# Kernel tuning notes

Measured on AMD Instinct MI355X. Metric: run time of the kernel, lower is better.

Reference implementation:

```python
import jax, jax.numpy as jnp
import numpy as np

N_NODES = 50000
N_EDGES = 600000
DIM = 128
N_HEADS = 3
EDGE_VOCAB = 22754
NEG_SLOPE = 0.2


def setup_inputs() -> dict:
    key = jax.random.key(0)
    ks = jax.random.split(key, 12)
    s = 1.0 / np.sqrt(DIM)
    return {
        "x": jax.random.normal(ks[0], (N_NODES, DIM), dtype=jnp.float32),
        "edge_index": jax.random.randint(ks[1], (2, N_EDGES), 0, N_NODES, dtype=jnp.int64),
        "edge_ids": jax.random.randint(ks[2], (N_EDGES,), 0, EDGE_VOCAB, dtype=jnp.int64),
        "ddi_weight": jax.random.uniform(ks[3], (N_EDGES,), dtype=jnp.float32),
        "W_lin": jax.random.normal(ks[4], (DIM, DIM), dtype=jnp.float32) * s,
        "b_lin": jnp.zeros((DIM,), dtype=jnp.float32),
        "edge_emb": jax.random.normal(ks[5], (EDGE_VOCAB, 1), dtype=jnp.float32) * 0.1,
        "W_heads": jax.random.normal(ks[6], (N_HEADS, DIM, DIM), dtype=jnp.float32) * s,
        "att_src": jax.random.normal(ks[7], (N_HEADS, DIM), dtype=jnp.float32) * s,
        "att_dst": jax.random.normal(ks[8], (N_HEADS, DIM), dtype=jnp.float32) * s,
        "bias_heads": jnp.zeros((N_HEADS, DIM), dtype=jnp.float32),
    }


def _gat_head(x, src, dst, ew, W, a_src, a_dst, bias):
    # x: [N, D] (already passed through shared lin), ew: [E] scalar edge weights
    h = x @ W                                   # [N, D]
    e = jax.nn.leaky_relu(
        (h @ a_src)[src] + (h @ a_dst)[dst], NEG_SLOPE)   # [E]
    # segment softmax over destination nodes
    e_max = jax.ops.segment_max(e, dst, num_segments=N_NODES)   # [N]
    e_exp = jnp.exp(e - e_max[dst])                              # [E]
    denom = jax.ops.segment_sum(e_exp, dst, num_segments=N_NODES)
    alpha = e_exp / jnp.maximum(denom[dst], 1e-16)               # [E]
    msg = (alpha * ew)[:, None] * h[src]                         # [E, D]
    return jax.ops.segment_sum(msg, dst, num_segments=N_NODES) + bias


def reference(x, edge_index, edge_ids, ddi_weight, W_lin, b_lin, edge_emb,
              W_heads, att_src, att_dst, bias_heads):
    x = x @ W_lin + b_lin                         # shared linear projection
    ew = edge_emb[edge_ids, 0] - ddi_weight        # [E]
    src, dst = edge_index[0], edge_index[1]
    out = jnp.zeros_like(x)
    for hix in range(N_HEADS):                     # small fixed head count
        out = out + _gat_head(x, src, dst, ew, W_heads[hix],
                              att_src[hix], att_dst[hix], bias_heads[hix])
    return out / N_HEADS
```

## Files before the change

### kernel.cpp

```cpp
#include <hip/hip_runtime.h>
#include <math.h>

#define NN 50000
#define NE 600000
#define D 128
#define NH 3
#define CAP 64
#define EDGE_BLOCKS ((NE + 255) / 256)
#define MFMA_BLOCKS ((NN + 63) / 64)

typedef short bf16x8 __attribute__((ext_vector_type(8)));
typedef _Float16 f16x8 __attribute__((ext_vector_type(8)));
typedef float f32x4 __attribute__((ext_vector_type(4)));

__device__ __forceinline__ unsigned short f2b(float f) {
  unsigned int u = __float_as_uint(f);
  u += 0x7FFF + ((u >> 16) & 1);
  return (unsigned short)(u >> 16);
}
__device__ __forceinline__ float blo(unsigned int u) {
  return __uint_as_float(u << 16);
}
__device__ __forceinline__ float bhi(unsigned int u) {
  return __uint_as_float(u & 0xffff0000u);
}
__device__ __forceinline__ unsigned short f2h(float f) {
  _Float16 t = (_Float16)f;
  return *(unsigned short*)&t;
}

__global__ __launch_bounds__(256) void pack_scatter2(const float* __restrict__ W_lin,
                                                     const float* __restrict__ W_heads,
                                                     const float* __restrict__ att_src,
                                                     const float* __restrict__ att_dst,
                                                     const float* __restrict__ b_lin,
                                                     const float* __restrict__ bias_heads,
                                                     const int* __restrict__ ei,
                                                     const int* __restrict__ eid,
                                                     const float* __restrict__ ddi,
                                                     const float* __restrict__ emb,
                                                     uint4* __restrict__ Bpack,
                                                     uint4* __restrict__ Wpack3,
                                                     float* __restrict__ sbuf,
                                                     float* __restrict__ bcomb2,
                                                     int* __restrict__ counts,
                                                     unsigned int* __restrict__ slots8) {
  const int bx = blockIdx.x;
  const int tid = threadIdx.x;
  if (bx < EDGE_BLOCKS) {
    int e = bx * 256 + tid;
    if (e < NE) {
      int src = ei[e], dst = ei[NE + e];
      int idx = atomicAdd(&counts[dst], 1);
      idx = idx < CAP ? idx : CAP - 1;
      float ew = emb[eid[e]] - ddi[e];
      slots8[dst * CAP + idx] = (unsigned int)src | ((unsigned int)f2b(ew) << 16);
    }
    return;
  }
  const int pb = bx - EDGE_BLOCKS;
  if (pb < 8) {
    int r = pb * 256 + tid;
    int nt = r >> 8, s = (r >> 6) & 3, q = (r >> 4) & 3, n0 = r & 15;
    int kbase = s * 32 + q * 8;
    int n = nt * 16 + n0;
    unsigned int w[4];
    #pragma unroll
    for (int p = 0; p < 4; ++p) {
      unsigned short lo = f2b(W_lin[(kbase + 2 * p) * D + n]);
      unsigned short hi = f2b(W_lin[(kbase + 2 * p + 1) * D + n]);
      w[p] = (unsigned int)lo | ((unsigned int)hi << 16);
    }
    Bpack[r] = make_uint4(w[0], w[1], w[2], w[3]);
  } else if (pb < 32) {
    int u = (pb - 8) * 256 + tid;
    int h = u >> 11, r = u & 2047;
    int nt = r >> 8, s = (r >> 6) & 3, q = (r >> 4) & 3, n0 = r & 15;
    int kbase = s * 32 + q * 8;
    int n = nt * 16 + n0;
    const float* W = W_heads + (size_t)h * D * D;
    unsigned int w[4];
    #pragma unroll
    for (int p = 0; p < 4; ++p) {
      unsigned short lo = f2h(W[(kbase + 2 * p) * D + n]);
      unsigned short hi = f2h(W[(kbase + 2 * p + 1) * D + n]);
      w[p] = (unsigned int)lo | ((unsigned int)hi << 16);
    }
    Wpack3[h * 2048 + r] = make_uint4(w[0], w[1], w[2], w[3]);
  } else if (pb < 35) {
    const int h = pb - 32;
    __shared__ float wha_s[128], wha_d[128], scs[128], scd[128];
    {
      int m = tid & 127;
      const float* W = W_heads + (size_t)h * D * D + m * D;
      const float* a = (tid < 128) ? (att_src + h * D) : (att_dst + h * D);
      float acc = 0.f;
      for (int n = 0; n < D; ++n) acc += W[n] * a[n];
      if (tid < 128) wha_s[m] = acc; else wha_d[m] = acc;
    }
    __syncthreads();
    {
      int k = tid & 127;
      const float* wl = W_lin + k * D;
      const float* wha = (tid < 128) ? wha_s : wha_d;
      float acc = 0.f;
      for (int m = 0; m < D; ++m) acc += wl[m] * wha[m];
      if (tid < 128) scs[k] = acc; else scd[k] = acc;
    }
    __syncthreads();
    if (tid < 2) {
      const float* wha = tid ? wha_d : wha_s;
      float a = 0.f;
      for (int k = 0; k < D; ++k) a += b_lin[k] * wha[k];
      sbuf[h * 2 + tid] = a;
    }
    {
      int s = (tid >> 6) & 3, q = (tid >> 4) & 3, n0 = tid & 15;
      int kbase = s * 32 + q * 8;
      bool mine = (n0 < 6) && ((n0 >> 1) == h);
      bool zero = (h == 0) && (n0 >= 6);
      if (mine || zero) {
        float vals[8];
        #pragma unroll
        for (int j = 0; j < 8; ++j)
          vals[j] = zero ? 0.f : ((n0 & 1) ? scd[kbase + j] : scs[kbase + j]);
        unsigned int w[4];
        #pragma unroll
        for (int p = 0; p < 4; ++p)
          w[p] = (unsigned int)f2b(vals[2 * p]) | ((unsigned int)f2b(vals[2 * p + 1]) << 16);
        Bpack[2048 + tid] = make_uint4(w[0], w[1], w[2], w[3]);
      }
    }
  } else {
    if (tid < D)
      bcomb2[tid] = (bias_heads[tid] + bias_heads[D + tid] + bias_heads[2 * D + tid]) * (1.f / 3.f);
  }
}

__global__ __launch_bounds__(256) void mfma_x(const float* __restrict__ x,
                                              const uint4* __restrict__ Bpack,
                                              const float* __restrict__ b_lin,
                                              const float* __restrict__ sbuf,
                                              unsigned short* __restrict__ xb,
                                              float* __restrict__ s_src4,
                                              float* __restrict__ s_dst4) {
  const int row0 = blockIdx.x * 64;
  const int tid = threadIdx.x;
  __shared__ __align__(16) unsigned short As[64][136];
  #pragma unroll
  for (int it = 0; it < 8; ++it) {
    int idx = tid + it * 256;
    int m = idx >> 5, k4 = idx & 31;
    int row = row0 + m;
    float4 v = make_float4(0.f, 0.f, 0.f, 0.f);
    if (row < NN) v = ((const float4*)(x + (size_t)row * D))[k4];
    uint2 pk;
    pk.x = (unsigned int)f2b(v.x) | ((unsigned int)f2b(v.y) << 16);
    pk.y = (unsigned int)f2b(v.z) | ((unsigned int)f2b(v.w) << 16);
    *((uint2*)&As[m][k4 * 4]) = pk;
  }
  __syncthreads();
  const int wv = tid >> 6;
  const int lane = tid & 63;
  const int n0 = lane & 15, q = lane >> 4;
  const int boff = q * 16 + n0;
  const bf16x8* Bp = (const bf16x8*)Bpack;

  bf16x8 a4[4];
  #pragma unroll
  for (int s = 0; s < 4; ++s)
    a4[s] = *(const bf16x8*)&As[wv * 16 + n0][s * 32 + q * 8];

  f32x4 acc[9];
  #pragma unroll
  for (int nt = 0; nt < 9; ++nt) acc[nt] = (f32x4){0.f, 0.f, 0.f, 0.f};

  #pragma unroll
  for (int s = 0; s < 4; ++s) {
    #pragma unroll
    for (int nt = 0; nt < 9; ++nt) {
      bf16x8 b = Bp[(nt * 4 + s) * 64 + boff];
      acc[nt] = __builtin_amdgcn_mfma_f32_16x16x32_bf16(a4[s], b, acc[nt], 0, 0, 0);
    }
  }
  __syncthreads();
  #pragma unroll
  for (int nt = 0; nt < 8; ++nt) {
    int col = nt * 16 + n0;
    float bv = b_lin[col];
    #pragma unroll
    for (int r = 0; r < 4; ++r)
      As[wv * 16 + q * 4 + r][col] = f2b(acc[nt][r] + bv);
  }
  if (n0 < 6) {
    float sb = sbuf[n0];
    float* Sout = (n0 & 1) ? s_dst4 : s_src4;
    #pragma unroll
    for (int r = 0; r < 4; ++r) {
      int row = row0 + wv * 16 + q * 4 + r;
      if (row < NN) Sout[row * 4 + (n0 >> 1)] = acc[8][r] + sb;
    }
  }
  __syncthreads();
  #pragma unroll
  for (int i = 0; i < 4; ++i) {
    int idx = tid + i * 256;
    int row = idx >> 4, c16 = idx & 15;
    int grow = row0 + row;
    if (grow < NN)
      *((uint4*)&xb[(size_t)grow * D + c16 * 8]) = *((const uint4*)&As[row][c16 * 8]);
  }
}

__global__ __launch_bounds__(512) void gfin(const int* __restrict__ counts,
                                            const unsigned int* __restrict__ slots8,
                                            const float4* __restrict__ s_src4,
                                            const float4* __restrict__ s_dst4,
                                            const unsigned short* __restrict__ xb,
                                            const uint4* __restrict__ Wpack3,
                                            const float* __restrict__ bcomb2,
                                            float* __restrict__ out) {
  const int row0 = blockIdx.x * 64;
  const int tid = threadIdx.x;
  const int wv = tid >> 6;
  const int lane = tid & 63;
  __shared__ __align__(16) _Float16 Acc[64][392];

  const int hf = lane >> 5;
  const int c = (lane & 31) * 4;
  for (int i = 0; i < 8; ++i) {
    const int m = wv * 8 + i;
    const int dst = row0 + m;
    if (dst < NN) {
      int cnt = counts[dst];
      cnt = cnt < CAP ? cnt : CAP;
      const int beg = dst * CAP;
      const int end = beg + cnt;
      float4 sd = s_dst4[dst];
      float a0[4] = {0.f, 0.f, 0.f, 0.f};
      float a1[4] = {0.f, 0.f, 0.f, 0.f};
      float a2[4] = {0.f, 0.f, 0.f, 0.f};
      float d0 = 0.f, d1 = 0.f, d2 = 0.f;
      int s = beg + hf;
      for (; s + 2 < end; s += 4) {
        unsigned int seA = slots8[s];
        unsigned int seB = slots8[s + 2];
        int srcA = seA & 0xffffu, srcB = seB & 0xffffu;
        float ewA = bhi(seA), ewB = bhi(seB);
        float4 ssA = s_src4[srcA];
        float4 ssB = s_src4[srcB];
        uint2 ua = *(const uint2*)&xb[(size_t)srcA * D + c];
        uint2 ub = *(const uint2*)&xb[(size_t)srcB * D + c];
        float vA0 = ssA.x + sd.x, vA1 = ssA.y + sd.y, vA2 = ssA.z + sd.z;
        float vB0 = ssB.x + sd.x, vB1 = ssB.y + sd.y, vB2 = ssB.z + sd.z;
        vA0 = vA0 > 0.f ? vA0 : 0.2f * vA0;
        vA1 = vA1 > 0.f ? vA1 : 0.2f * vA1;
        vA2 = vA2 > 0.f ? vA2 : 0.2f * vA2;
        vB0 = vB0 > 0.f ? vB0 : 0.2f * vB0;
        vB1 = vB1 > 0.f ? vB1 : 0.2f * vB1;
        vB2 = vB2 > 0.f ? vB2 : 0.2f * vB2;
        float pA0 = __expf(vA0), pA1 = __expf(vA1), pA2 = __expf(vA2);
        float pB0 = __expf(vB0), pB1 = __expf(vB1), pB2 = __expf(vB2);
        float wa0 = pA0 * ewA, wa1 = pA1 * ewA, wa2 = pA2 * ewA;
        float wb0 = pB0 * ewB, wb1 = pB1 * ewB, wb2 = pB2 * ewB;
        float xA[4] = {blo(ua.x), bhi(ua.x), blo(ua.y), bhi(ua.y)};
        float xB[4] = {blo(ub.x), bhi(ub.x), blo(ub.y), bhi(ub.y)};
        #pragma unroll
        for (int j = 0; j < 4; ++j) {
          a0[j] += wa0 * xA[j] + wb0 * xB[j];
          a1[j] += wa1 * xA[j] + wb1 * xB[j];
          a2[j] += wa2 * xA[j] + wb2 * xB[j];
        }
        d0 += pA0 + pB0;
        d1 += pA1 + pB1;
        d2 += pA2 + pB2;
      }
      if (s < end) {
        unsigned int seA = slots8[s];
        int srcA = seA & 0xffffu;
        float ewA = bhi(seA);
        float4 ssA = s_src4[srcA];
        uint2 ua = *(const uint2*)&xb[(size_t)srcA * D + c];
        float vA0 = ssA.x + sd.x, vA1 = ssA.y + sd.y, vA2 = ssA.z + sd.z;
        vA0 = vA0 > 0.f ? vA0 : 0.2f * vA0;
        vA1 = vA1 > 0.f ? vA1 : 0.2f * vA1;
        vA2 = vA2 > 0.f ? vA2 : 0.2f * vA2;
        float pA0 = __expf(vA0), pA1 = __expf(vA1), pA2 = __expf(vA2);
        float w0 = pA0 * ewA, w1 = pA1 * ewA, w2 = pA2 * ewA;
        float xA[4] = {blo(ua.x), bhi(ua.x), blo(ua.y), bhi(ua.y)};
        #pragma unroll
        for (int j = 0; j < 4; ++j) {
          a0[j] += w0 * xA[j];
          a1[j] += w1 * xA[j];
          a2[j] += w2 * xA[j];
        }
        d0 += pA0; d1 += pA1; d2 += pA2;
      }
      #pragma unroll
      for (int j = 0; j < 4; ++j) {
        a0[j] += __shfl_xor(a0[j], 32, 64);
        a1[j] += __shfl_xor(a1[j], 32, 64);
        a2[j] += __shfl_xor(a2[j], 32, 64);
      }
      d0 += __shfl_xor(d0, 32, 64);
      d1 += __shfl_xor(d1, 32, 64);
      d2 += __shfl_xor(d2, 32, 64);
      if (hf == 0) {
        float r0 = 1.f / (3.f * fmaxf(d0, 1e-16f));
        float r1 = 1.f / (3.f * fmaxf(d1, 1e-16f));
        float r2 = 1.f / (3.f * fmaxf(d2, 1e-16f));
        uint2 o;
        o.x = (unsigned int)f2h(a0[0] * r0) | ((unsigned int)f2h(a0[1] * r0) << 16);
        o.y = (unsigned int)f2h(a0[2] * r0) | ((unsigned int)f2h(a0[3] * r0) << 16);
        *(uint2*)&Acc[m][c] = o;
        o.x = (unsigned int)f2h(a1[0] * r1) | ((unsigned int)f2h(a1[1] * r1) << 16);
        o.y = (unsigned int)f2h(a1[2] * r1) | ((unsigned int)f2h(a1[3] * r1) << 16);
        *(uint2*)&Acc[m][D + c] = o;
        o.x = (unsigned int)f2h(a2[0] * r2) | ((unsigned int)f2h(a2[1] * r2) << 16);
        o.y = (unsigned int)f2h(a2[2] * r2) | ((unsigned int)f2h(a2[3] * r2) << 16);
        *(uint2*)&Acc[m][2 * D + c] = o;
      }
    }
  }
  __syncthreads();

  const int n0 = lane & 15, q = lane >> 4;
  const int rw = wv & 3;
  const int cb = wv >> 2;
  const int boff = q * 16 + n0;
  f32x4 o4[4];
  #pragma unroll
  for (int nt = 0; nt < 4; ++nt) o4[nt] = (f32x4){0.f, 0.f, 0.f, 0.f};

  #pragma unroll
  for (int ck = 0; ck < NH; ++ck) {
    f16x8 af[4];
    #pragma unroll
    for (int s = 0; s < 4; ++s)
      af[s] = *(const f16x8*)&Acc[rw * 16 + n0][ck * D + s * 32 + q * 8];
    const f16x8* Bp = (const f16x8*)(Wpack3 + ck * 2048);
    #pragma unroll
    for (int s = 0; s < 4; ++s) {
      #pragma unroll
      for (int nt = 0; nt < 4; ++nt) {
        int NT = cb * 4 + nt;
        f16x8 b = Bp[(NT * 4 + s) * 64 + boff];
        o4[nt] = __builtin_amdgcn_mfma_f32_16x16x32_f16(af[s], b, o4[nt], 0, 0, 0);
      }
    }
  }
  #pragma unroll
  for (int nt = 0; nt < 4; ++nt) {
    int col = cb * 64 + nt * 16 + n0;
    float bv = bcomb2[col];
    #pragma unroll
    for (int r = 0; r < 4; ++r) {
      int row = row0 + rw * 16 + q * 4 + r;
      if (row < NN) out[(size_t)row * D + col] = o4[nt][r] + bv;
    }
  }
}

extern "C" void kernel_launch(void* const* d_in, const int* in_sizes, int n_in,
                              void* d_out, int out_size, void* d_ws, size_t ws_size,
                              hipStream_t stream) {
  const float* x          = (const float*)d_in[0];
  const int*   ei         = (const int*)d_in[1];
  const int*   eid        = (const int*)d_in[2];
  const float* ddi        = (const float*)d_in[3];
  const float* W_lin      = (const float*)d_in[4];
  const float* b_lin      = (const float*)d_in[5];
  const float* emb        = (const float*)d_in[6];
  const float* W_heads    = (const float*)d_in[7];
  const float* att_src    = (const float*)d_in[8];
  const float* att_dst    = (const float*)d_in[9];
  const float* bias_heads = (const float*)d_in[10];
  float* out = (float*)d_out;

  uint4*  Bpack  = (uint4*)d_ws;
  uint4*  Wpack3 = Bpack + 2304;
  unsigned short* xb = (unsigned short*)(Wpack3 + NH * 2048);
  unsigned int* slots8 = (unsigned int*)(xb + (size_t)NN * D);
  float*  sbuf   = (float*)(slots8 + (size_t)NN * CAP);
  float*  bcomb2 = sbuf + 8;
  float*  s_src4 = bcomb2 + 128;
  float*  s_dst4 = s_src4 + (size_t)NN * 4;
  int*    counts = (int*)(s_dst4 + (size_t)NN * 4);

  hipMemsetAsync(counts, 0, (size_t)NN * sizeof(int), stream);
  pack_scatter2<<<EDGE_BLOCKS + 36, 256, 0, stream>>>(
      W_lin, W_heads, att_src, att_dst, b_lin, bias_heads, ei, eid, ddi, emb,
      Bpack, Wpack3, sbuf, bcomb2, counts, slots8);
  mfma_x<<<MFMA_BLOCKS, 256, 0, stream>>>(x, Bpack, b_lin, sbuf, xb,
                                          s_src4, s_dst4);
  gfin<<<MFMA_BLOCKS, 512, 0, stream>>>(counts, slots8, (const float4*)s_src4,
                                        (const float4*)s_dst4, xb, Wpack3,
                                        bcomb2, out);
}
```

Baseline: 242.3 us.

## Split fused gather+GEMM into per-node gather kernel and separate MFMA GEMM

Splits the fused gather-and-project kernel into two kernels. The first is a one-wavefront-per-destination gather that writes per-head aggregated features as fp16 to global memory. The second is a tiled MFMA GEMM that reads those features back and applies the combined weights. It also folds log2(e) into the attention score weights so the kernel can use exp2f instead of __expf. The aim is better load balance and occupancy for the irregular gather, at the cost of an extra global round trip of about 38 MB for the intermediate features and one more launch.

```diff
diff --git a/kernel.cpp b/kernel.cpp
--- a/kernel.cpp
+++ b/kernel.cpp
@@ -8,6 +8,7 @@
 #define CAP 64
 #define EDGE_BLOCKS ((NE + 255) / 256)
 #define MFMA_BLOCKS ((NN + 63) / 64)
+#define LOG2E 1.44269504088896340736f
 
 typedef short bf16x8 __attribute__((ext_vector_type(8)));
 typedef _Float16 f16x8 __attribute__((ext_vector_type(8)));
@@ -105,14 +106,14 @@
       const float* wha = (tid < 128) ? wha_s : wha_d;
       float acc = 0.f;
       for (int m = 0; m < D; ++m) acc += wl[m] * wha[m];
-      if (tid < 128) scs[k] = acc; else scd[k] = acc;
+      if (tid < 128) scs[k] = acc * LOG2E; else scd[k] = acc * LOG2E;
     }
     __syncthreads();
     if (tid < 2) {
       const float* wha = tid ? wha_d : wha_s;
       float a = 0.f;
       for (int k = 0; k < D; ++k) a += b_lin[k] * wha[k];
-      sbuf[h * 2 + tid] = a;
+      sbuf[h * 2 + tid] = a * LOG2E;
     }
     {
       int s = (tid >> 6) & 3, q = (tid >> 4) & 3, n0 = tid & 15;
@@ -212,151 +213,158 @@
   }
 }
 
-__global__ __launch_bounds__(512) void gfin(const int* __restrict__ counts,
-                                            const unsigned int* __restrict__ slots8,
-                                            const float4* __restrict__ s_src4,
-                                            const float4* __restrict__ s_dst4,
-                                            const unsigned short* __restrict__ xb,
-                                            const uint4* __restrict__ Wpack3,
-                                            const float* __restrict__ bcomb2,
-                                            float* __restrict__ out) {
+__global__ __launch_bounds__(64) void gather12(const int* __restrict__ counts,
+                                               const unsigned int* __restrict__ slots8,
+                                               const float4* __restrict__ s_src4,
+                                               const float4* __restrict__ s_dst4,
+                                               const unsigned short* __restrict__ xb,
+                                               unsigned short* __restrict__ accb) {
+  const int dst = blockIdx.x;
+  const int lane = threadIdx.x;
+  const int hf = lane >> 5;
+  const int c = (lane & 31) * 4;
+  int cnt = counts[dst];
+  cnt = cnt < CAP ? cnt : CAP;
+  const int beg = dst * CAP;
+  const int end = beg + cnt;
+  float4 sd = s_dst4[dst];
+  float a0[4] = {0.f, 0.f, 0.f, 0.f};
+  float a1[4] = {0.f, 0.f, 0.f, 0.f};
+  float a2[4] = {0.f, 0.f, 0.f, 0.f};
+  float d0 = 0.f, d1 = 0.f, d2 = 0.f;
+  int s = beg + hf;
+  for (; s + 2 < end; s += 4) {
+    unsigned int seA = slots8[s];
+    unsigned int seB = slots8[s + 2];
+    int srcA = seA & 0xffffu, srcB = seB & 0xffffu;
+    float ewA = bhi(seA), ewB = bhi(seB);
+    float4 ssA = s_src4[srcA];
+    float4 ssB = s_src4[srcB];
+    uint2 ua = *(const uint2*)&xb[(size_t)srcA * D + c];
+    uint2 ub = *(const uint2*)&xb[(size_t)srcB * D + c];
+    float vA0 = ssA.x + sd.x, vA1 = ssA.y + sd.y, vA2 = ssA.z + sd.z;
+    float vB0 = ssB.x + sd.x, vB1 = ssB.y + sd.y, vB2 = ssB.z + sd.z;
+    vA0 = vA0 > 0.f ? vA0 : 0.2f * vA0;
+    vA1 = vA1 > 0.f ? vA1 : 0.2f * vA1;
+    vA2 = vA2 > 0.f ? vA2 : 0.2f * vA2;
+    vB0 = vB0 > 0.f ? vB0 : 0.2f * vB0;
+    vB1 = vB1 > 0.f ? vB1 : 0.2f * vB1;
+    vB2 = vB2 > 0.f ? vB2 : 0.2f * vB2;
+    float pA0 = exp2f(vA0), pA1 = exp2f(vA1), pA2 = exp2f(vA2);
+    float pB0 = exp2f(vB0), pB1 = exp2f(vB1), pB2 = exp2f(vB2);
+    float wa0 = pA0 * ewA, wa1 = pA1 * ewA, wa2 = pA2 * ewA;
+    float wb0 = pB0 * ewB, wb1 = pB1 * ewB, wb2 = pB2 * ewB;
+    float xA[4] = {blo(ua.x), bhi(ua.x), blo(ua.y), bhi(ua.y)};
+    float xB[4] = {blo(ub.x), bhi(ub.x), blo(ub.y), bhi(ub.y)};
+    #pragma unroll
+    for (int j = 0; j < 4; ++j) {
+      a0[j] += wa0 * xA[j] + wb0 * xB[j];
+      a1[j] += wa1 * xA[j] + wb1 * xB[j];
+      a2[j] += wa2 * xA[j] + wb2 * xB[j];
+    }
+    d0 += pA0 + pB0;
+    d1 += pA1 + pB1;
+    d2 += pA2 + pB2;
+  }
+  if (s < end) {
+    unsigned int seA = slots8[s];
+    int srcA = seA & 0xffffu;
+    float ewA = bhi(seA);
+    float4 ssA = s_src4[srcA];
+    uint2 ua = *(const uint2*)&xb[(size_t)srcA * D + c];
+    float vA0 = ssA.x + sd.x, vA1 = ssA.y + sd.y, vA2 = ssA.z + sd.z;
+    vA0 = vA0 > 0.f ? vA0 : 0.2f * vA0;
+    vA1 = vA1 > 0.f ? vA1 : 0.2f * vA1;
+    vA2 = vA2 > 0.f ? vA2 : 0.2f * vA2;
+    float pA0 = exp2f(vA0), pA1 = exp2f(vA1), pA2 = exp2f(vA2);
+    float w0 = pA0 * ewA, w1 = pA1 * ewA, w2 = pA2 * ewA;
+    float xA[4] = {blo(ua.x), bhi(ua.x), blo(ua.y), bhi(ua.y)};
+    #pragma unroll
+    for (int j = 0; j < 4; ++j) {
+      a0[j] += w0 * xA[j];
+      a1[j] += w1 * xA[j];
+      a2[j] += w2 * xA[j];
+    }
+    d0 += pA0; d1 += pA1; d2 += pA2;
+  }
+  #pragma unroll
+  for (int j = 0; j < 4; ++j) {
+    a0[j] += __shfl_xor(a0[j], 32, 64);
+    a1[j] += __shfl_xor(a1[j], 32, 64);
+    a2[j] += __shfl_xor(a2[j], 32, 64);
+  }
+  d0 += __shfl_xor(d0, 32, 64);
+  d1 += __shfl_xor(d1, 32, 64);
+  d2 += __shfl_xor(d2, 32, 64);
+  if (hf == 0) {
+    float r0 = 1.f / (3.f * fmaxf(d0, 1e-16f));
+    float r1 = 1.f / (3.f * fmaxf(d1, 1e-16f));
+    float r2 = 1.f / (3.f * fmaxf(d2, 1e-16f));
+    unsigned short* base = accb + (size_t)dst * (NH * D);
+    uint2 o;
+    o.x = (unsigned int)f2h(a0[0] * r0) | ((unsigned int)f2h(a0[1] * r0) << 16);
+    o.y = (unsigned int)f2h(a0[2] * r0) | ((unsigned int)f2h(a0[3] * r0) << 16);
+    *(uint2*)&base[c] = o;
+    o.x = (unsigned int)f2h(a1[0] * r1) | ((unsigned int)f2h(a1[1] * r1) << 16);
+    o.y = (unsigned int)f2h(a1[2] * r1) | ((unsigned int)f2h(a1[3] * r1) << 16);
+    *(uint2*)&base[D + c] = o;
+    o.x = (unsigned int)f2h(a2[0] * r2) | ((unsigned int)f2h(a2[1] * r2) << 16);
+    o.y = (unsigned int)f2h(a2[2] * r2) | ((unsigned int)f2h(a2[3] * r2) << 16);
+    *(uint2*)&base[2 * D + c] = o;
+  }
+}
+
+__global__ __launch_bounds__(256) void final_gemm16(const unsigned short* __restrict__ accb,
+                                                    const uint4* __restrict__ Wpack3,
+                                                    const float* __restrict__ bcomb2,
+                                                    float* __restrict__ out) {
   const int row0 = blockIdx.x * 64;
   const int tid = threadIdx.x;
+  __shared__ __align__(16) _Float16 Af[64][136];
   const int wv = tid >> 6;
   const int lane = tid & 63;
-  __shared__ __align__(16) _Float16 Acc[64][392];
-
-  const int hf = lane >> 5;
-  const int c = (lane & 31) * 4;
-  for (int i = 0; i < 8; ++i) {
-    const int m = wv * 8 + i;
-    const int dst = row0 + m;
-    if (dst < NN) {
-      int cnt = counts[dst];
-      cnt = cnt < CAP ? cnt : CAP;
-      const int beg = dst * CAP;
-      const int end = beg + cnt;
-      float4 sd = s_dst4[dst];
-      float a0[4] = {0.f, 0.f, 0.f, 0.f};
-      float a1[4] = {0.f, 0.f, 0.f, 0.f};
-      float a2[4] = {0.f, 0.f, 0.f, 0.f};
-      float d0 = 0.f, d1 = 0.f, d2 = 0.f;
-      int s = beg + hf;
-      for (; s + 2 < end; s += 4) {
-        unsigned int seA = slots8[s];
-        unsigned int seB = slots8[s + 2];
-        int srcA = seA & 0xffffu, srcB = seB & 0xffffu;
-        float ewA = bhi(seA), ewB = bhi(seB);
-        float4 ssA = s_src4[srcA];
-        float4 ssB = s_src4[srcB];
-        uint2 ua = *(const uint2*)&xb[(size_t)srcA * D + c];
-        uint2 ub = *(const uint2*)&xb[(size_t)srcB * D + c];
-        float vA0 = ssA.x + sd.x, vA1 = ssA.y + sd.y, vA2 = ssA.z + sd.z;
-        float vB0 = ssB.x + sd.x, vB1 = ssB.y + sd.y, vB2 = ssB.z + sd.z;
-        vA0 = vA0 > 0.f ? vA0 : 0.2f * vA0;
-        vA1 = vA1 > 0.f ? vA1 : 0.2f * vA1;
-        vA2 = vA2 > 0.f ? vA2 : 0.2f * vA2;
-        vB0 = vB0 > 0.f ? vB0 : 0.2f * vB0;
-        vB1 = vB1 > 0.f ? vB1 : 0.2f * vB1;
-        vB2 = vB2 > 0.f ? vB2 : 0.2f * vB2;
-        float pA0 = __expf(vA0), pA1 = __expf(vA1), pA2 = __expf(vA2);
-        float pB0 = __expf(vB0), pB1 = __expf(vB1), pB2 = __expf(vB2);
-        float wa0 = pA0 * ewA, wa1 = pA1 * ewA, wa2 = pA2 * ewA;
-        float wb0 = pB0 * ewB, wb1 = pB1 * ewB, wb2 = pB2 * ewB;
-        float xA[4] = {blo(ua.x), bhi(ua.x), blo(ua.y), bhi(ua.y)};
-        float xB[4] = {blo(ub.x), bhi(ub.x), blo(ub.y), bhi(ub.y)};
-        #pragma unroll
-        for (int j = 0; j < 4; ++j) {
-          a0[j] += wa0 * xA[j] + wb0 * xB[j];
-          a1[j] += wa1 * xA[j] + wb1 * xB[j];
-          a2[j] += wa2 * xA[j] + wb2 * xB[j];
-        }
-        d0 += pA0 + pB0;
-        d1 += pA1 + pB1;
-        d2 += pA2 + pB2;
-      }
-      if (s < end) {
-        unsigned int seA = slots8[s];
-        int srcA = seA & 0xffffu;
-        float ewA = bhi(seA);
-        float4 ssA = s_src4[srcA];
-        uint2 ua = *(const uint2*)&xb[(size_t)srcA * D + c];
-        float vA0 = ssA.x + sd.x, vA1 = ssA.y + sd.y, vA2 = ssA.z + sd.z;
-        vA0 = vA0 > 0.f ? vA0 : 0.2f * vA0;
-        vA1 = vA1 > 0.f ? vA1 : 0.2f * vA1;
-        vA2 = vA2 > 0.f ? vA2 : 0.2f * vA2;
-        float pA0 = __expf(vA0), pA1 = __expf(vA1), pA2 = __expf(vA2);
-        float w0 = pA0 * ewA, w1 = pA1 * ewA, w2 = pA2 * ewA;
-        float xA[4] = {blo(ua.x), bhi(ua.x), blo(ua.y), bhi(ua.y)};
-        #pragma unroll
-        for (int j = 0; j < 4; ++j) {
-          a0[j] += w0 * xA[j];
-          a1[j] += w1 * xA[j];
-          a2[j] += w2 * xA[j];
-        }
-        d0 += pA0; d1 += pA1; d2 += pA2;
-      }
-      #pragma unroll
-      for (int j = 0; j < 4; ++j) {
-        a0[j] += __shfl_xor(a0[j], 32, 64);
-        a1[j] += __shfl_xor(a1[j], 32, 64);
-        a2[j] += __shfl_xor(a2[j], 32, 64);
-      }
-      d0 += __shfl_xor(d0, 32, 64);
-      d1 += __shfl_xor(d1, 32, 64);
-      d2 += __shfl_xor(d2, 32, 64);
-      if (hf == 0) {
-        float r0 = 1.f / (3.f * fmaxf(d0, 1e-16f));
-        float r1 = 1.f / (3.f * fmaxf(d1, 1e-16f));
-        float r2 = 1.f / (3.f * fmaxf(d2, 1e-16f));
-        uint2 o;
-        o.x = (unsigned int)f2h(a0[0] * r0) | ((unsigned int)f2h(a0[1] * r0) << 16);
-        o.y = (unsigned int)f2h(a0[2] * r0) | ((unsigned int)f2h(a0[3] * r0) << 16);
-        *(uint2*)&Acc[m][c] = o;
-        o.x = (unsigned int)f2h(a1[0] * r1) | ((unsigned int)f2h(a1[1] * r1) << 16);
-        o.y = (unsigned int)f2h(a1[2] * r1) | ((unsigned int)f2h(a1[3] * r1) << 16);
-        *(uint2*)&Acc[m][D + c] = o;
-        o.x = (unsigned int)f2h(a2[0] * r2) | ((unsigned int)f2h(a2[1] * r2) << 16);
-        o.y = (unsigned int)f2h(a2[2] * r2) | ((unsigned int)f2h(a2[3] * r2) << 16);
-        *(uint2*)&Acc[m][2 * D + c] = o;
-      }
-    }
-  }
-  __syncthreads();
-
   const int n0 = lane & 15, q = lane >> 4;
-  const int rw = wv & 3;
-  const int cb = wv >> 2;
   const int boff = q * 16 + n0;
-  f32x4 o4[4];
-  #pragma unroll
-  for (int nt = 0; nt < 4; ++nt) o4[nt] = (f32x4){0.f, 0.f, 0.f, 0.f};
-
-  #pragma unroll
+
+  f32x4 o[8];
+  #pragma unroll
+  for (int nt = 0; nt < 8; ++nt) o[nt] = (f32x4){0.f, 0.f, 0.f, 0.f};
+
   for (int ck = 0; ck < NH; ++ck) {
+    if (ck) __syncthreads();
+    #pragma unroll
+    for (int it = 0; it < 4; ++it) {
+      int idx = tid + it * 256;
+      int m = idx >> 4, k8 = idx & 15;
+      int row = row0 + m;
+      uint4 u = make_uint4(0, 0, 0, 0);
+      if (row < NN)
+        u = *(const uint4*)&accb[(size_t)row * (NH * D) + ck * D + k8 * 8];
+      *((uint4*)&Af[m][k8 * 8]) = u;
+    }
+    __syncthreads();
     f16x8 af[4];
     #pragma unroll
     for (int s = 0; s < 4; ++s)
-      af[s] = *(const f16x8*)&Acc[rw * 16 + n0][ck * D + s * 32 + q * 8];
+      af[s] = *(const f16x8*)&Af[wv * 16 + n0][s * 32 + q * 8];
     const f16x8* Bp = (const f16x8*)(Wpack3 + ck * 2048);
     #pragma unroll
     for (int s = 0; s < 4; ++s) {
       #pragma unroll
-      for (int nt = 0; nt < 4; ++nt) {
-        int NT = cb * 4 + nt;
-        f16x8 b = Bp[(NT * 4 + s) * 64 + boff];
-        o4[nt] = __builtin_amdgcn_mfma_f32_16x16x32_f16(af[s], b, o4[nt], 0, 0, 0);
+      for (int nt = 0; nt < 8; ++nt) {
+        f16x8 b = Bp[(nt * 4 + s) * 64 + boff];
+        o[nt] = __builtin_amdgcn_mfma_f32_16x16x32_f16(af[s], b, o[nt], 0, 0, 0);
       }
     }
   }
   #pragma unroll
-  for (int nt = 0; nt < 4; ++nt) {
-    int col = cb * 64 + nt * 16 + n0;
+  for (int nt = 0; nt < 8; ++nt) {
+    int col = nt * 16 + n0;
     float bv = bcomb2[col];
     #pragma unroll
     for (int r = 0; r < 4; ++r) {
-      int row = row0 + rw * 16 + q * 4 + r;
-      if (row < NN) out[(size_t)row * D + col] = o4[nt][r] + bv;
+      int row = row0 + wv * 16 + q * 4 + r;
+      if (row < NN) out[(size_t)row * D + col] = o[nt][r] + bv;
     }
   }
 }
@@ -381,7 +389,8 @@
   uint4*  Wpack3 = Bpack + 2304;
   unsigned short* xb = (unsigned short*)(Wpack3 + NH * 2048);
   unsigned int* slots8 = (unsigned int*)(xb + (size_t)NN * D);
-  float*  sbuf   = (float*)(slots8 + (size_t)NN * CAP);
+  unsigned short* accb = (unsigned short*)(slots8 + (size_t)NN * CAP);
+  float*  sbuf   = (float*)(accb + (size_t)NN * NH * D);
   float*  bcomb2 = sbuf + 8;
   float*  s_src4 = bcomb2 + 128;
   float*  s_dst4 = s_src4 + (size_t)NN * 4;
@@ -393,7 +402,7 @@
       Bpack, Wpack3, sbuf, bcomb2, counts, slots8);
   mfma_x<<<MFMA_BLOCKS, 256, 0, stream>>>(x, Bpack, b_lin, sbuf, xb,
                                           s_src4, s_dst4);
-  gfin<<<MFMA_BLOCKS, 512, 0, stream>>>(counts, slots8, (const float4*)s_src4,
-                                        (const float4*)s_dst4, xb, Wpack3,
-                                        bcomb2, out);
-}
+  gather12<<<NN, 64, 0, stream>>>(counts, slots8, (const float4*)s_src4,
+                                  (const float4*)s_dst4, xb, accb);
+  final_gemm16<<<MFMA_BLOCKS, 256, 0, stream>>>(accb, Wpack3, bcomb2, out);
+}
```

New measurement: 215.5 us. 1.12x faster.
